# Kernel tuning notes

Hardware: AMD Instinct MI355X
Metric: run time of the kernel (lower is better)

Reference implementation:

```python
import jax, jax.numpy as jnp
import numpy as np

B, H, Wd, C = 32, 32, 32, 128
N = H * Wd  # flattened spatial dim = Dense units per channel


def setup_inputs() -> dict:
    key = jax.random.key(0)
    k1, k2 = jax.random.split(key)
    inputs = jax.random.normal(k1, (B, H, Wd, C), dtype=jnp.float32)
    # Per-channel Dense weights stacked: [C, N, N], glorot-ish scale
    W = jax.random.normal(k2, (C, N, N), dtype=jnp.float32) * (1.0 / np.sqrt(N))
    b = jnp.zeros((C, N), dtype=jnp.float32)
    return {"inputs": inputs, "W": W, "b": b}


def reference(inputs, W, b):
    Bb, h, w, c = inputs.shape
    n = h * w
    x = inputs.reshape(Bb, n, c)                      # [B, N, C]
    # one batched GEMM over channels instead of C separate Dense calls
    y = jnp.einsum('bnc,cnm->bcm', x, W) + b          # [B, C, N]
    y = jax.nn.relu(y)
    y = y.reshape(Bb, c, h, w).transpose(0, 2, 3, 1)  # [B, H, W, C]
    # original concatenates each new channel at the FRONT -> reversed channel order
    return y[..., ::-1]
```

## Files before the change

### kernel.cpp

```cpp
#include <hip/hip_runtime.h>

#define Bb 32
#define NN 1024
#define CC 128
#define KS 64
#define MT 128

typedef __bf16 bf16x8 __attribute__((ext_vector_type(8)));
typedef float f32x16 __attribute__((ext_vector_type(16)));
typedef float f32x4 __attribute__((ext_vector_type(4)));
typedef unsigned short u16x4 __attribute__((ext_vector_type(4)));
typedef unsigned short u16x8 __attribute__((ext_vector_type(8)));

__device__ __forceinline__ unsigned short f2bf(float f) {
    unsigned u = __builtin_bit_cast(unsigned, f);
    u = (u + 0x7FFFu + ((u >> 16) & 1u)) >> 16;
    return (unsigned short)u;
}

__global__ __launch_bounds__(256) void transpose_x(const float* __restrict__ in,
                                                   unsigned short* __restrict__ xbf) {
    __shared__ float tile[64 * 132];
    const int b  = blockIdx.x >> 4;
    const int n0 = (blockIdx.x & 15) << 6;
    const int t  = threadIdx.x;

#pragma unroll
    for (int p = 0; p < 8; ++p) {
        int f     = p * 256 + t;
        int n_off = f >> 5;
        int c4    = (f & 31) << 2;
        f32x4 v = *reinterpret_cast<const f32x4*>(in + ((size_t)(b * NN + n0 + n_off) * CC + c4));
        *reinterpret_cast<f32x4*>(&tile[n_off * 132 + c4]) = v;
    }
    __syncthreads();

    const int c = t >> 1, half = t & 1;
    const size_t obase = ((size_t)c * Bb + b) * NN + n0;
#pragma unroll
    for (int q = 0; q < 4; ++q) {
        int nb = half * 32 + q * 8;
        u16x8 o;
#pragma unroll
        for (int j = 0; j < 8; ++j) o[j] = f2bf(tile[(nb + j) * 132 + c]);
        *reinterpret_cast<u16x8*>(xbf + obase + nb) = o;
    }
}

template <int USE_XBF>
__global__ __launch_bounds__(256) void cwdense(const float* __restrict__ W,
                                               const float* __restrict__ bias,
                                               const float* __restrict__ xin,
                                               const unsigned short* __restrict__ xbf,
                                               float* __restrict__ out) {
    __shared__ unsigned short wlds[MT * KS];

    const int x     = blockIdx.x;
    const int xcd   = x & 7;
    const int i     = x >> 3;
    const int c     = xcd * 16 + (i & 15);
    const int mtile = i >> 4;
    const int m0    = mtile * MT;

    const int t    = threadIdx.x;
    const int w    = t >> 6;
    const int lane = t & 63;
    const int lm   = lane & 31;
    const int lh   = lane >> 5;
    const int m_loc = w * 32 + lm;

    const float* wpanel = W + (size_t)c * NN * NN + m0;

    const int mq  = t & 31;
    const int kq2 = t >> 5;

    f32x16 acc;
#pragma unroll
    for (int r = 0; r < 16; ++r) acc[r] = 0.0f;

    for (int step = 0; step < NN / KS; ++step) {
        const int k0 = step * KS;

        f32x4 q[2][4];
#pragma unroll
        for (int qi = 0; qi < 2; ++qi)
#pragma unroll
            for (int r = 0; r < 4; ++r)
                q[qi][r] = *reinterpret_cast<const f32x4*>(
                    wpanel + (size_t)(k0 + (kq2 * 2 + qi) * 4 + r) * NN + mq * 4);

        __syncthreads();

#pragma unroll
        for (int qi = 0; qi < 2; ++qi) {
            const int kkbase = (kq2 * 2 + qi) * 4;
#pragma unroll
            for (int j = 0; j < 4; ++j) {
                const int m = mq * 4 + j;
                u16x4 o;
#pragma unroll
                for (int r = 0; r < 4; ++r) o[r] = f2bf(q[qi][r][j]);
                const int slot = (kkbase >> 3) ^ (m & 7) ^ ((m >> 3) & 7);
                *reinterpret_cast<u16x4*>(&wlds[m * 64 + slot * 8 + (kkbase & 7)]) = o;
            }
        }
        __syncthreads();

#pragma unroll
        for (int mi = 0; mi < 4; ++mi) {
            const int kk = mi * 16 + lh * 8;
            bf16x8 a;
            if (USE_XBF) {
                a = *reinterpret_cast<const bf16x8*>(
                    xbf + ((size_t)(c * Bb + lm) * NN + k0 + kk));
            } else {
                u16x8 tmp;
#pragma unroll
                for (int e = 0; e < 8; ++e)
                    tmp[e] = f2bf(xin[((size_t)lm * NN + (k0 + kk + e)) * CC + c]);
                a = __builtin_bit_cast(bf16x8, tmp);
            }
            const int slot = (kk >> 3) ^ (m_loc & 7) ^ ((m_loc >> 3) & 7);
            bf16x8 bf = *reinterpret_cast<const bf16x8*>(&wlds[m_loc * 64 + slot * 8]);
            acc = __builtin_amdgcn_mfma_f32_32x32x16_bf16(a, bf, acc, 0, 0, 0);
        }
    }

    const int m  = m0 + m_loc;
    const float bv = bias[(size_t)c * NN + m];
    const int co = (CC - 1) - c;
#pragma unroll
    for (int r = 0; r < 16; ++r) {
        const int brow = (r & 3) + 8 * (r >> 2) + 4 * lh;
        float v = acc[r] + bv;
        v = v > 0.0f ? v : 0.0f;
        out[(size_t)brow * (NN * CC) + (size_t)m * CC + co] = v;
    }
}

extern "C" void kernel_launch(void* const* d_in, const int* in_sizes, int n_in,
                              void* d_out, int out_size, void* d_ws, size_t ws_size,
                              hipStream_t stream) {
    const float* xinp = (const float*)d_in[0];
    const float* W    = (const float*)d_in[1];
    const float* bias = (const float*)d_in[2];
    float* out        = (float*)d_out;

    const size_t need = (size_t)CC * Bb * NN * sizeof(unsigned short);
    if (ws_size >= need) {
        unsigned short* xbf = (unsigned short*)d_ws;
        transpose_x<<<512, 256, 0, stream>>>(xinp, xbf);
        cwdense<1><<<1024, 256, 0, stream>>>(W, bias, xinp, xbf, out);
    } else {
        cwdense<0><<<1024, 256, 0, stream>>>(W, bias, xinp, nullptr, out);
    }
}
```

Before: 134.7 us.

## Double-buffer W tile register prefetch and use native bf16 conversion

Global loads of W for the next two K-steps are issued into two register buffers (qA/qB) ahead of use, so load latency overlaps with LDS stores and MFMA work. The manual round-to-nearest bf16 conversion is replaced by the native __bf16 cast, which may lower to a hardware convert instruction. It also adds a launch-bounds occupancy hint of 4 blocks. This doubles the per-thread register footprint for prefetched tiles, which could lower occupancy or cause spills.

```diff
diff --git a/kernel.cpp b/kernel.cpp
--- a/kernel.cpp
+++ b/kernel.cpp
@@ -7,19 +7,13 @@
 #define MT 128
 
 typedef __bf16 bf16x8 __attribute__((ext_vector_type(8)));
+typedef __bf16 bf16x4 __attribute__((ext_vector_type(4)));
 typedef float f32x16 __attribute__((ext_vector_type(16)));
 typedef float f32x4 __attribute__((ext_vector_type(4)));
-typedef unsigned short u16x4 __attribute__((ext_vector_type(4)));
 typedef unsigned short u16x8 __attribute__((ext_vector_type(8)));
 
-__device__ __forceinline__ unsigned short f2bf(float f) {
-    unsigned u = __builtin_bit_cast(unsigned, f);
-    u = (u + 0x7FFFu + ((u >> 16) & 1u)) >> 16;
-    return (unsigned short)u;
-}
-
 __global__ __launch_bounds__(256) void transpose_x(const float* __restrict__ in,
-                                                   unsigned short* __restrict__ xbf) {
+                                                   __bf16* __restrict__ xbf) {
     __shared__ float tile[64 * 132];
     const int b  = blockIdx.x >> 4;
     const int n0 = (blockIdx.x & 15) << 6;
@@ -40,20 +34,20 @@
 #pragma unroll
     for (int q = 0; q < 4; ++q) {
         int nb = half * 32 + q * 8;
-        u16x8 o;
+        bf16x8 o;
 #pragma unroll
-        for (int j = 0; j < 8; ++j) o[j] = f2bf(tile[(nb + j) * 132 + c]);
-        *reinterpret_cast<u16x8*>(xbf + obase + nb) = o;
+        for (int j = 0; j < 8; ++j) o[j] = (__bf16)tile[(nb + j) * 132 + c];
+        *reinterpret_cast<bf16x8*>(xbf + obase + nb) = o;
     }
 }
 
 template <int USE_XBF>
-__global__ __launch_bounds__(256) void cwdense(const float* __restrict__ W,
-                                               const float* __restrict__ bias,
-                                               const float* __restrict__ xin,
-                                               const unsigned short* __restrict__ xbf,
-                                               float* __restrict__ out) {
-    __shared__ unsigned short wlds[MT * KS];
+__global__ __launch_bounds__(256, 4) void cwdense(const float* __restrict__ W,
+                                                  const float* __restrict__ bias,
+                                                  const float* __restrict__ xin,
+                                                  const __bf16* __restrict__ xbf,
+                                                  float* __restrict__ out) {
+    __shared__ __bf16 wlds[MT * 64];
 
     const int x     = blockIdx.x;
     const int xcd   = x & 7;
@@ -78,34 +72,33 @@
 #pragma unroll
     for (int r = 0; r < 16; ++r) acc[r] = 0.0f;
 
-    for (int step = 0; step < NN / KS; ++step) {
-        const int k0 = step * KS;
+    f32x4 qA[8], qB[8];
 
-        f32x4 q[2][4];
+    auto load_tile = [&](f32x4 (&q)[8], int k0) {
 #pragma unroll
-        for (int qi = 0; qi < 2; ++qi)
-#pragma unroll
-            for (int r = 0; r < 4; ++r)
-                q[qi][r] = *reinterpret_cast<const f32x4*>(
-                    wpanel + (size_t)(k0 + (kq2 * 2 + qi) * 4 + r) * NN + mq * 4);
+        for (int r = 0; r < 8; ++r) {
+            const int kk = (kq2 * 2 + (r >> 2)) * 4 + (r & 3);
+            q[r] = *reinterpret_cast<const f32x4*>(wpanel + (size_t)(k0 + kk) * NN + mq * 4);
+        }
+    };
 
-        __syncthreads();
-
+    auto store_tile = [&](const f32x4 (&q)[8]) {
 #pragma unroll
         for (int qi = 0; qi < 2; ++qi) {
             const int kkbase = (kq2 * 2 + qi) * 4;
 #pragma unroll
             for (int j = 0; j < 4; ++j) {
                 const int m = mq * 4 + j;
-                u16x4 o;
+                bf16x4 o;
 #pragma unroll
-                for (int r = 0; r < 4; ++r) o[r] = f2bf(q[qi][r][j]);
+                for (int r = 0; r < 4; ++r) o[r] = (__bf16)q[qi * 4 + r][j];
                 const int slot = (kkbase >> 3) ^ (m & 7) ^ ((m >> 3) & 7);
-                *reinterpret_cast<u16x4*>(&wlds[m * 64 + slot * 8 + (kkbase & 7)]) = o;
+                *reinterpret_cast<bf16x4*>(&wlds[m * 64 + slot * 8 + (kkbase & 7)]) = o;
             }
         }
-        __syncthreads();
+    };
 
+    auto mfma_step = [&](int k0) {
 #pragma unroll
         for (int mi = 0; mi < 4; ++mi) {
             const int kk = mi * 16 + lh * 8;
@@ -116,14 +109,36 @@
             } else {
                 u16x8 tmp;
 #pragma unroll
-                for (int e = 0; e < 8; ++e)
-                    tmp[e] = f2bf(xin[((size_t)lm * NN + (k0 + kk + e)) * CC + c]);
+                for (int e = 0; e < 8; ++e) {
+                    float f = xin[((size_t)lm * NN + (k0 + kk + e)) * CC + c];
+                    unsigned u = __builtin_bit_cast(unsigned, f);
+                    u = (u + 0x7FFFu + ((u >> 16) & 1u)) >> 16;
+                    tmp[e] = (unsigned short)u;
+                }
                 a = __builtin_bit_cast(bf16x8, tmp);
             }
             const int slot = (kk >> 3) ^ (m_loc & 7) ^ ((m_loc >> 3) & 7);
-            bf16x8 bf = *reinterpret_cast<const bf16x8*>(&wlds[m_loc * 64 + slot * 8]);
-            acc = __builtin_amdgcn_mfma_f32_32x32x16_bf16(a, bf, acc, 0, 0, 0);
+            bf16x8 bfrag = *reinterpret_cast<const bf16x8*>(&wlds[m_loc * 64 + slot * 8]);
+            acc = __builtin_amdgcn_mfma_f32_32x32x16_bf16(a, bfrag, acc, 0, 0, 0);
         }
+    };
+
+    load_tile(qA, 0);
+    load_tile(qB, KS);
+
+#pragma unroll 1
+    for (int s = 0; s < NN / KS; s += 2) {
+        __syncthreads();
+        store_tile(qA);
+        if (s + 2 < NN / KS) load_tile(qA, (s + 2) * KS);
+        __syncthreads();
+        mfma_step(s * KS);
+
+        __syncthreads();
+        store_tile(qB);
+        if (s + 3 < NN / KS) load_tile(qB, (s + 3) * KS);
+        __syncthreads();
+        mfma_step((s + 1) * KS);
     }
 
     const int m  = m0 + m_loc;
@@ -146,9 +161,9 @@
     const float* bias = (const float*)d_in[2];
     float* out        = (float*)d_out;
 
-    const size_t need = (size_t)CC * Bb * NN * sizeof(unsigned short);
+    const size_t need = (size_t)CC * Bb * NN * sizeof(__bf16);
     if (ws_size >= need) {
-        unsigned short* xbf = (unsigned short*)d_ws;
+        __bf16* xbf = (__bf16*)d_ws;
         transpose_x<<<512, 256, 0, stream>>>(xinp, xbf);
         cwdense<1><<<1024, 256, 0, stream>>>(W, bias, xinp, xbf, out);
     } else {
```

After: 143.4 us. +6.4%, slower.
